# Optimization experiments

Measured on AMD Instinct MI355X. Metric: run time of the kernel, lower is better.

Reference implementation:

```python
import jax, jax.numpy as jnp
import numpy as np

N_NODES = 50000
N_EDGES = 400000
IN_DIM = 128
HID_DIM = 128
OUT_DIM = 128


def setup_inputs() -> dict:
    key = jax.random.key(0)
    k_x, k_e, k_w1, k_b1, k_w2, k_b2 = jax.random.split(key, 6)
    x = jax.random.normal(k_x, (N_NODES, IN_DIM), dtype=jnp.float32)
    edge_index = jax.random.randint(k_e, (2, N_EDGES), 0, N_NODES, dtype=jnp.int64)
    # nn.Linear-style params: W is [out, in], kaiming-uniform-ish init
    lim1 = 1.0 / np.sqrt(IN_DIM)
    lim2 = 1.0 / np.sqrt(HID_DIM)
    W1 = jax.random.uniform(k_w1, (HID_DIM, IN_DIM), jnp.float32, -lim1, lim1)
    b1 = jax.random.uniform(k_b1, (HID_DIM,), jnp.float32, -lim1, lim1)
    W2 = jax.random.uniform(k_w2, (OUT_DIM, HID_DIM), jnp.float32, -lim2, lim2)
    b2 = jax.random.uniform(k_b2, (OUT_DIM,), jnp.float32, -lim2, lim2)
    return {"x": x, "edge_index": edge_index, "W1": W1, "b1": b1, "W2": W2, "b2": b2}


def reference(x, edge_index, W1, b1, W2, b2):
    # h = relu(fc1(x));  dropout in eval mode -> identity
    h = jax.nn.relu(x @ W1.T + b1)                      # [N, hid]
    src, dst = edge_index[0], edge_index[1]
    # gather messages from src, scatter-add (mean) into dst
    agg = jax.ops.segment_sum(h[src], dst, num_segments=N_NODES)      # [N, hid]
    deg = jax.ops.segment_sum(jnp.ones_like(dst, dtype=h.dtype), dst,
                              num_segments=N_NODES)                   # [N]
    deg = jnp.maximum(deg, 1.0)
    agg = agg / deg[:, None]
    # residual add + fc2
    return (agg + h) @ W2.T + b2                        # [N, out]
```

## Files before the change

kernel.cpp:

```cpp
#include <hip/hip_runtime.h>

#define N_NODES 50000
#define N_EDGES 400000
#define DIM 128
#define N_SCAN_BLK ((N_NODES + 255) / 256)

typedef unsigned short u16;
typedef unsigned int   u32;
typedef __bf16 v8bf  __attribute__((ext_vector_type(8)));
typedef float  f32x4 __attribute__((ext_vector_type(4)));
typedef u16    u16x8 __attribute__((ext_vector_type(8)));

union BF8 { u16x8 u; v8bf b; };

__device__ __forceinline__ float bf2f(u16 u) {
    union { u32 i; float f; } v; v.i = ((u32)u) << 16; return v.f;
}
__device__ __forceinline__ u16 f2bf(float f) {
    union { float f; u32 i; } v; v.f = f; u32 u = v.i;
    return (u16)((u + 0x7FFFu + ((u >> 16) & 1u)) >> 16);
}

__global__ __launch_bounds__(256) void cast_w_kernel(
    const float* __restrict__ W1, const float* __restrict__ W2,
    u16* __restrict__ Wb1, u16* __restrict__ Wb2)
{
    int i = blockIdx.x * 256 + threadIdx.x;
    if (i < DIM * DIM) {
        Wb1[i] = f2bf(W1[i]);
        Wb2[i] = f2bf(W2[i]);
    }
}

__global__ __launch_bounds__(256, 3) void fc1_mfma(
    const float* __restrict__ x, const u16* __restrict__ Wb,
    const float* __restrict__ b, u16* __restrict__ h)
{
    __shared__ u16 xs[64 * 136];
    const int t = threadIdx.x;
    const int wave = t >> 6, lane = t & 63, quad = lane >> 4, l15 = lane & 15;
    const int ch = wave >> 1, rh = wave & 1;
    const int row0 = blockIdx.x * 64;

    BF8 barr[4][4];
#pragma unroll
    for (int ct = 0; ct < 4; ++ct)
#pragma unroll
        for (int ks = 0; ks < 4; ++ks)
            barr[ct][ks].u = *(const u16x8*)(
                Wb + (size_t)(ch * 64 + ct * 16 + l15) * DIM + ks * 32 + quad * 8);

    {
        int srow = t >> 2, k0 = (t & 3) * 32;
        int grow = row0 + srow; if (grow >= N_NODES) grow = N_NODES - 1;
        const float* xp = x + (size_t)grow * DIM + k0;
#pragma unroll
        for (int j = 0; j < 4; ++j) {
            float4 f0 = *(const float4*)(xp + j * 8);
            float4 f1 = *(const float4*)(xp + j * 8 + 4);
            u16x8 p;
            p[0] = f2bf(f0.x); p[1] = f2bf(f0.y); p[2] = f2bf(f0.z); p[3] = f2bf(f0.w);
            p[4] = f2bf(f1.x); p[5] = f2bf(f1.y); p[6] = f2bf(f1.z); p[7] = f2bf(f1.w);
            *(u16x8*)&xs[srow * 136 + k0 + j * 8] = p;
        }
    }

    f32x4 acc[2][4];
#pragma unroll
    for (int ct = 0; ct < 4; ++ct) {
        float bv = b[ch * 64 + ct * 16 + l15];
        acc[0][ct] = (f32x4){bv, bv, bv, bv};
        acc[1][ct] = (f32x4){bv, bv, bv, bv};
    }
    __syncthreads();

#pragma unroll
    for (int ks = 0; ks < 4; ++ks) {
        BF8 a0, a1;
        a0.u = *(const u16x8*)&xs[(rh * 32 +  0 + l15) * 136 + ks * 32 + quad * 8];
        a1.u = *(const u16x8*)&xs[(rh * 32 + 16 + l15) * 136 + ks * 32 + quad * 8];
#pragma unroll
        for (int ct = 0; ct < 4; ++ct) {
            acc[0][ct] = __builtin_amdgcn_mfma_f32_16x16x32_bf16(
                a0.b, barr[ct][ks].b, acc[0][ct], 0, 0, 0);
            acc[1][ct] = __builtin_amdgcn_mfma_f32_16x16x32_bf16(
                a1.b, barr[ct][ks].b, acc[1][ct], 0, 0, 0);
        }
    }

#pragma unroll
    for (int rt = 0; rt < 2; ++rt)
#pragma unroll
        for (int i = 0; i < 4; ++i) {
            int row = row0 + rh * 32 + rt * 16 + quad * 4 + i;
            if (row < N_NODES) {
#pragma unroll
                for (int ct = 0; ct < 4; ++ct) {
                    int col = ch * 64 + ct * 16 + l15;
                    h[(size_t)row * DIM + col] = f2bf(fmaxf(acc[rt][ct][i], 0.f));
                }
            }
        }
}

__global__ __launch_bounds__(256, 3) void fc2_mfma(
    const u16* __restrict__ z, const u16* __restrict__ Wb,
    const float* __restrict__ b, float* __restrict__ out)
{
    __shared__ u16 xs[64 * 136];
    const int t = threadIdx.x;
    const int wave = t >> 6, lane = t & 63, quad = lane >> 4, l15 = lane & 15;
    const int ch = wave >> 1, rh = wave & 1;
    const int row0 = blockIdx.x * 64;

    BF8 barr[4][4];
#pragma unroll
    for (int ct = 0; ct < 4; ++ct)
#pragma unroll
        for (int ks = 0; ks < 4; ++ks)
            barr[ct][ks].u = *(const u16x8*)(
                Wb + (size_t)(ch * 64 + ct * 16 + l15) * DIM + ks * 32 + quad * 8);

    {
        int srow = t >> 1, k0 = (t & 1) * 64;
        int grow = row0 + srow; if (grow >= N_NODES) grow = N_NODES - 1;
        const u16* zp = z + (size_t)grow * DIM + k0;
#pragma unroll
        for (int j = 0; j < 8; ++j)
            *(u16x8*)&xs[srow * 136 + k0 + j * 8] = *(const u16x8*)(zp + j * 8);
    }

    f32x4 acc[2][4];
#pragma unroll
    for (int ct = 0; ct < 4; ++ct) {
        float bv = b[ch * 64 + ct * 16 + l15];
        acc[0][ct] = (f32x4){bv, bv, bv, bv};
        acc[1][ct] = (f32x4){bv, bv, bv, bv};
    }
    __syncthreads();

#pragma unroll
    for (int ks = 0; ks < 4; ++ks) {
        BF8 a0, a1;
        a0.u = *(const u16x8*)&xs[(rh * 32 +  0 + l15) * 136 + ks * 32 + quad * 8];
        a1.u = *(const u16x8*)&xs[(rh * 32 + 16 + l15) * 136 + ks * 32 + quad * 8];
#pragma unroll
        for (int ct = 0; ct < 4; ++ct) {
            acc[0][ct] = __builtin_amdgcn_mfma_f32_16x16x32_bf16(
                a0.b, barr[ct][ks].b, acc[0][ct], 0, 0, 0);
            acc[1][ct] = __builtin_amdgcn_mfma_f32_16x16x32_bf16(
                a1.b, barr[ct][ks].b, acc[1][ct], 0, 0, 0);
        }
    }

#pragma unroll
    for (int rt = 0; rt < 2; ++rt)
#pragma unroll
        for (int i = 0; i < 4; ++i) {
            int row = row0 + rh * 32 + rt * 16 + quad * 4 + i;
            if (row < N_NODES) {
#pragma unroll
                for (int ct = 0; ct < 4; ++ct) {
                    int col = ch * 64 + ct * 16 + l15;
                    out[(size_t)row * DIM + col] = acc[rt][ct][i];
                }
            }
        }
}

__global__ __launch_bounds__(256) void count_kernel(
    const int* __restrict__ edst, int* __restrict__ counts)
{
    int e = blockIdx.x * 256 + threadIdx.x;
    if (e >= N_EDGES) return;
    int dst = edst[e];
    if ((unsigned)dst >= N_NODES) return;
    atomicAdd(&counts[dst], 1);
}

__global__ __launch_bounds__(256) void scan_blocks_kernel(
    const int* __restrict__ counts, int* __restrict__ row_ptr,
    int* __restrict__ bsum)
{
    __shared__ int tmp[256];
    const int t = threadIdx.x;
    const int i = blockIdx.x * 256 + t;
    int v = (i < N_NODES) ? counts[i] : 0;
    tmp[t] = v;
    __syncthreads();
#pragma unroll
    for (int ofs = 1; ofs < 256; ofs <<= 1) {
        int add = (t >= ofs) ? tmp[t - ofs] : 0;
        __syncthreads();
        tmp[t] += add;
        __syncthreads();
    }
    if (i < N_NODES) row_ptr[i] = tmp[t] - v;
    if (t == 255) bsum[blockIdx.x] = tmp[255];
}

__global__ __launch_bounds__(256) void scan_top_kernel(
    const int* __restrict__ bsum, int* __restrict__ boff)
{
    __shared__ int tmp[256];
    const int t = threadIdx.x;
    int v = (t < N_SCAN_BLK) ? bsum[t] : 0;
    tmp[t] = v;
    __syncthreads();
#pragma unroll
    for (int ofs = 1; ofs < 256; ofs <<= 1) {
        int add = (t >= ofs) ? tmp[t - ofs] : 0;
        __syncthreads();
        tmp[t] += add;
        __syncthreads();
    }
    if (t < N_SCAN_BLK) boff[t] = tmp[t] - v;
}

__global__ __launch_bounds__(256) void scan_fixup_kernel(
    const int* __restrict__ boff, int* __restrict__ row_ptr,
    int* __restrict__ cursor)
{
    int i = blockIdx.x * 256 + threadIdx.x;
    if (i < N_NODES) {
        int r = row_ptr[i] + boff[blockIdx.x];
        row_ptr[i] = r;
        cursor[i]  = r;
    }
    if (i == 0) row_ptr[N_NODES] = N_EDGES;
}

__global__ __launch_bounds__(256) void bucket_kernel(
    const int* __restrict__ esrc, const int* __restrict__ edst,
    int* __restrict__ cursor, int* __restrict__ esorted)
{
    int e = blockIdx.x * 256 + threadIdx.x;
    if (e >= N_EDGES) return;
    int src = esrc[e], dst = edst[e];
    if ((unsigned)src >= N_NODES || (unsigned)dst >= N_NODES) return;
    int pos = atomicAdd(&cursor[dst], 1);
    esorted[pos] = src;
}

__global__ __launch_bounds__(64) void aggregate_kernel(
    const int* __restrict__ row_ptr, const int* __restrict__ esorted,
    const u16* __restrict__ h, u16* __restrict__ z)
{
    const int n = blockIdx.x;
    const int t = threadIdx.x;
    const int start = row_ptr[n];
    const int end   = row_ptr[n + 1];

    float a0 = 0.f, a1 = 0.f;
    int e = start;
    for (; e + 4 <= end; e += 4) {
        int s0 = esorted[e + 0];
        int s1 = esorted[e + 1];
        int s2 = esorted[e + 2];
        int s3 = esorted[e + 3];
        u32 v0 = *(const u32*)(h + (size_t)s0 * DIM + t * 2);
        u32 v1 = *(const u32*)(h + (size_t)s1 * DIM + t * 2);
        u32 v2 = *(const u32*)(h + (size_t)s2 * DIM + t * 2);
        u32 v3 = *(const u32*)(h + (size_t)s3 * DIM + t * 2);
        a0 += bf2f((u16)v0); a1 += bf2f((u16)(v0 >> 16));
        a0 += bf2f((u16)v1); a1 += bf2f((u16)(v1 >> 16));
        a0 += bf2f((u16)v2); a1 += bf2f((u16)(v2 >> 16));
        a0 += bf2f((u16)v3); a1 += bf2f((u16)(v3 >> 16));
    }
    for (; e < end; ++e) {
        u32 v = *(const u32*)(h + (size_t)esorted[e] * DIM + t * 2);
        a0 += bf2f((u16)v); a1 += bf2f((u16)(v >> 16));
    }

    int deg = end - start;
    float inv = (deg > 0) ? 1.f / (float)deg : 1.f;
    u32 r = *(const u32*)(h + (size_t)n * DIM + t * 2);
    float z0 = a0 * inv + bf2f((u16)r);
    float z1 = a1 * inv + bf2f((u16)(r >> 16));
    u32 p = (u32)f2bf(z0) | ((u32)f2bf(z1) << 16);
    *(u32*)(z + (size_t)n * DIM + t * 2) = p;
}

extern "C" void kernel_launch(void* const* d_in, const int* in_sizes, int n_in,
                              void* d_out, int out_size, void* d_ws, size_t ws_size,
                              hipStream_t stream)
{
    const float* x  = (const float*)d_in[0];
    const int*   ei = (const int*)d_in[1];
    const float* W1 = (const float*)d_in[2];
    const float* b1 = (const float*)d_in[3];
    const float* W2 = (const float*)d_in[4];
    const float* b2 = (const float*)d_in[5];
    float* out = (float*)d_out;

    const int* esrc = ei;
    const int* edst = ei + N_EDGES;

    char* ws = (char*)d_ws;
    size_t off = 0;
    u16* h        = (u16*)(ws + off); off += (size_t)N_NODES * DIM * 2;
    u16* z        = (u16*)(ws + off); off += (size_t)N_NODES * DIM * 2;
    u16* Wb1      = (u16*)(ws + off); off += (size_t)DIM * DIM * 2;
    u16* Wb2      = (u16*)(ws + off); off += (size_t)DIM * DIM * 2;
    int* counts   = (int*)(ws + off); off += (size_t)N_NODES * 4;
    int* row_ptr  = (int*)(ws + off); off += (size_t)(N_NODES + 1) * 4;
    int* cursor   = (int*)(ws + off); off += (size_t)N_NODES * 4;
    int* esorted  = (int*)(ws + off); off += (size_t)N_EDGES * 4;
    int* bsum     = (int*)(ws + off); off += (size_t)N_SCAN_BLK * 4;
    int* boff     = (int*)(ws + off); off += (size_t)N_SCAN_BLK * 4;

    hipMemsetAsync(counts, 0, (size_t)N_NODES * 4, stream);
    cast_w_kernel<<<(DIM * DIM + 255) / 256, 256, 0, stream>>>(W1, W2, Wb1, Wb2);

    fc1_mfma<<<(N_NODES + 63) / 64, 256, 0, stream>>>(x, Wb1, b1, h);
    count_kernel<<<(N_EDGES + 255) / 256, 256, 0, stream>>>(edst, counts);
    scan_blocks_kernel<<<N_SCAN_BLK, 256, 0, stream>>>(counts, row_ptr, bsum);
    scan_top_kernel<<<1, 256, 0, stream>>>(bsum, boff);
    scan_fixup_kernel<<<N_SCAN_BLK, 256, 0, stream>>>(boff, row_ptr, cursor);
    bucket_kernel<<<(N_EDGES + 255) / 256, 256, 0, stream>>>(
        esrc, edst, cursor, esorted);
    aggregate_kernel<<<N_NODES, 64, 0, stream>>>(row_ptr, esorted, h, z);
    fc2_mfma<<<(N_NODES + 63) / 64, 256, 0, stream>>>(z, Wb2, b2, out);
}
```

Before: 181.9 us.

## Fuse CSR build into cooperative kernel and fuse aggregation into fc2

```diff
diff --git a/kernel.cpp b/kernel.cpp
--- a/kernel.cpp
+++ b/kernel.cpp
@@ -1,9 +1,13 @@
 #include <hip/hip_runtime.h>
+#include <hip/hip_cooperative_groups.h>
+
+namespace cg = cooperative_groups;
 
 #define N_NODES 50000
 #define N_EDGES 400000
 #define DIM 128
 #define N_SCAN_BLK ((N_NODES + 255) / 256)
+#define CSR_BLOCKS 512
 
 typedef unsigned short u16;
 typedef unsigned int   u32;
@@ -21,14 +25,82 @@
     return (u16)((u + 0x7FFFu + ((u >> 16) & 1u)) >> 16);
 }
 
-__global__ __launch_bounds__(256) void cast_w_kernel(
+__global__ __launch_bounds__(256) void csr_build(
+    const int* __restrict__ esrc, const int* __restrict__ edst,
     const float* __restrict__ W1, const float* __restrict__ W2,
-    u16* __restrict__ Wb1, u16* __restrict__ Wb2)
+    u16* __restrict__ Wb1, u16* __restrict__ Wb2,
+    int* __restrict__ counts, int* __restrict__ row_ptr,
+    int* __restrict__ cursor, int* __restrict__ esorted,
+    int* __restrict__ bsum, int* __restrict__ boff)
 {
-    int i = blockIdx.x * 256 + threadIdx.x;
-    if (i < DIM * DIM) {
+    cg::grid_group grid = cg::this_grid();
+    __shared__ int tmp[256];
+    const int t   = threadIdx.x;
+    const int bid = blockIdx.x;
+    const int gid = bid * 256 + t;
+    const int G   = CSR_BLOCKS * 256;
+
+    for (int i = gid; i < N_NODES; i += G) counts[i] = 0;
+    for (int i = gid; i < DIM * DIM; i += G) {
         Wb1[i] = f2bf(W1[i]);
         Wb2[i] = f2bf(W2[i]);
+    }
+    grid.sync();
+
+    for (int e = gid; e < N_EDGES; e += G) {
+        int dst = edst[e];
+        if ((unsigned)dst < N_NODES) atomicAdd(&counts[dst], 1);
+    }
+    grid.sync();
+
+    if (bid < N_SCAN_BLK) {
+        int i = bid * 256 + t;
+        int v = (i < N_NODES) ? counts[i] : 0;
+        tmp[t] = v;
+        __syncthreads();
+#pragma unroll
+        for (int ofs = 1; ofs < 256; ofs <<= 1) {
+            int add = (t >= ofs) ? tmp[t - ofs] : 0;
+            __syncthreads();
+            tmp[t] += add;
+            __syncthreads();
+        }
+        if (i < N_NODES) row_ptr[i] = tmp[t] - v;
+        if (t == 255) bsum[bid] = tmp[255];
+    }
+    grid.sync();
+
+    if (bid == 0) {
+        int v = (t < N_SCAN_BLK) ? bsum[t] : 0;
+        tmp[t] = v;
+        __syncthreads();
+#pragma unroll
+        for (int ofs = 1; ofs < 256; ofs <<= 1) {
+            int add = (t >= ofs) ? tmp[t - ofs] : 0;
+            __syncthreads();
+            tmp[t] += add;
+            __syncthreads();
+        }
+        if (t < N_SCAN_BLK) boff[t] = tmp[t] - v;
+    }
+    grid.sync();
+
+    if (bid < N_SCAN_BLK) {
+        int i = bid * 256 + t;
+        if (i < N_NODES) {
+            int r = row_ptr[i] + boff[bid];
+            row_ptr[i] = r;
+            cursor[i]  = r;
+        }
+        if (i == 0) row_ptr[N_NODES] = N_EDGES;
+    }
+    grid.sync();
+
+    for (int e = gid; e < N_EDGES; e += G) {
+        int src = esrc[e], dst = edst[e];
+        if ((unsigned)src >= N_NODES || (unsigned)dst >= N_NODES) continue;
+        int pos = atomicAdd(&cursor[dst], 1);
+        esorted[pos] = src;
     }
 }
 
@@ -103,11 +175,12 @@
         }
 }
 
-__global__ __launch_bounds__(256, 3) void fc2_mfma(
-    const u16* __restrict__ z, const u16* __restrict__ Wb,
+__global__ __launch_bounds__(256, 3) void agg_fc2(
+    const int* __restrict__ row_ptr, const int* __restrict__ esorted,
+    const u16* __restrict__ h, const u16* __restrict__ Wb,
     const float* __restrict__ b, float* __restrict__ out)
 {
-    __shared__ u16 xs[64 * 136];
+    __shared__ u16 zs[64 * 136];
     const int t = threadIdx.x;
     const int wave = t >> 6, lane = t & 63, quad = lane >> 4, l15 = lane & 15;
     const int ch = wave >> 1, rh = wave & 1;
@@ -121,13 +194,41 @@
             barr[ct][ks].u = *(const u16x8*)(
                 Wb + (size_t)(ch * 64 + ct * 16 + l15) * DIM + ks * 32 + quad * 8);
 
-    {
-        int srow = t >> 1, k0 = (t & 1) * 64;
-        int grow = row0 + srow; if (grow >= N_NODES) grow = N_NODES - 1;
-        const u16* zp = z + (size_t)grow * DIM + k0;
-#pragma unroll
-        for (int j = 0; j < 8; ++j)
-            *(u16x8*)&xs[srow * 136 + k0 + j * 8] = *(const u16x8*)(zp + j * 8);
+    for (int i = 0; i < 16; ++i) {
+        int srow = wave * 16 + i;
+        int n = row0 + srow;
+        u32 p = 0;
+        if (n < N_NODES) {
+            const int start = row_ptr[n];
+            const int end   = row_ptr[n + 1];
+            float a0 = 0.f, a1 = 0.f;
+            int e = start;
+            for (; e + 4 <= end; e += 4) {
+                int s0 = esorted[e + 0];
+                int s1 = esorted[e + 1];
+                int s2 = esorted[e + 2];
+                int s3 = esorted[e + 3];
+                u32 v0 = *(const u32*)(h + (size_t)s0 * DIM + lane * 2);
+                u32 v1 = *(const u32*)(h + (size_t)s1 * DIM + lane * 2);
+                u32 v2 = *(const u32*)(h + (size_t)s2 * DIM + lane * 2);
+                u32 v3 = *(const u32*)(h + (size_t)s3 * DIM + lane * 2);
+                a0 += bf2f((u16)v0); a1 += bf2f((u16)(v0 >> 16));
+                a0 += bf2f((u16)v1); a1 += bf2f((u16)(v1 >> 16));
+                a0 += bf2f((u16)v2); a1 += bf2f((u16)(v2 >> 16));
+                a0 += bf2f((u16)v3); a1 += bf2f((u16)(v3 >> 16));
+            }
+            for (; e < end; ++e) {
+                u32 v = *(const u32*)(h + (size_t)esorted[e] * DIM + lane * 2);
+                a0 += bf2f((u16)v); a1 += bf2f((u16)(v >> 16));
+            }
+            int deg = end - start;
+            float inv = (deg > 0) ? 1.f / (float)deg : 1.f;
+            u32 r = *(const u32*)(h + (size_t)n * DIM + lane * 2);
+            float z0 = a0 * inv + bf2f((u16)r);
+            float z1 = a1 * inv + bf2f((u16)(r >> 16));
+            p = (u32)f2bf(z0) | ((u32)f2bf(z1) << 16);
+        }
+        *(u32*)&zs[srow * 136 + lane * 2] = p;
     }
 
     f32x4 acc[2][4];
@@ -142,8 +243,8 @@
 #pragma unroll
     for (int ks = 0; ks < 4; ++ks) {
         BF8 a0, a1;
-        a0.u = *(const u16x8*)&xs[(rh * 32 +  0 + l15) * 136 + ks * 32 + quad * 8];
-        a1.u = *(const u16x8*)&xs[(rh * 32 + 16 + l15) * 136 + ks * 32 + quad * 8];
+        a0.u = *(const u16x8*)&zs[(rh * 32 +  0 + l15) * 136 + ks * 32 + quad * 8];
+        a1.u = *(const u16x8*)&zs[(rh * 32 + 16 + l15) * 136 + ks * 32 + quad * 8];
 #pragma unroll
         for (int ct = 0; ct < 4; ++ct) {
             acc[0][ct] = __builtin_amdgcn_mfma_f32_16x16x32_bf16(
@@ -166,119 +267,6 @@
                 }
             }
         }
-}
-
-__global__ __launch_bounds__(256) void count_kernel(
-    const int* __restrict__ edst, int* __restrict__ counts)
-{
-    int e = blockIdx.x * 256 + threadIdx.x;
-    if (e >= N_EDGES) return;
-    int dst = edst[e];
-    if ((unsigned)dst >= N_NODES) return;
-    atomicAdd(&counts[dst], 1);
-}
-
-__global__ __launch_bounds__(256) void scan_blocks_kernel(
-    const int* __restrict__ counts, int* __restrict__ row_ptr,
-    int* __restrict__ bsum)
-{
-    __shared__ int tmp[256];
-    const int t = threadIdx.x;
-    const int i = blockIdx.x * 256 + t;
-    int v = (i < N_NODES) ? counts[i] : 0;
-    tmp[t] = v;
-    __syncthreads();
-#pragma unroll
-    for (int ofs = 1; ofs < 256; ofs <<= 1) {
-        int add = (t >= ofs) ? tmp[t - ofs] : 0;
-        __syncthreads();
-        tmp[t] += add;
-        __syncthreads();
-    }
-    if (i < N_NODES) row_ptr[i] = tmp[t] - v;
-    if (t == 255) bsum[blockIdx.x] = tmp[255];
-}
-
-__global__ __launch_bounds__(256) void scan_top_kernel(
-    const int* __restrict__ bsum, int* __restrict__ boff)
-{
-    __shared__ int tmp[256];
-    const int t = threadIdx.x;
-    int v = (t < N_SCAN_BLK) ? bsum[t] : 0;
-    tmp[t] = v;
-    __syncthreads();
-#pragma unroll
-    for (int ofs = 1; ofs < 256; ofs <<= 1) {
-        int add = (t >= ofs) ? tmp[t - ofs] : 0;
-        __syncthreads();
-        tmp[t] += add;
-        __syncthreads();
-    }
-    if (t < N_SCAN_BLK) boff[t] = tmp[t] - v;
-}
-
-__global__ __launch_bounds__(256) void scan_fixup_kernel(
-    const int* __restrict__ boff, int* __restrict__ row_ptr,
-    int* __restrict__ cursor)
-{
-    int i = blockIdx.x * 256 + threadIdx.x;
-    if (i < N_NODES) {
-        int r = row_ptr[i] + boff[blockIdx.x];
-        row_ptr[i] = r;
-        cursor[i]  = r;
-    }
-    if (i == 0) row_ptr[N_NODES] = N_EDGES;
-}
-
-__global__ __launch_bounds__(256) void bucket_kernel(
-    const int* __restrict__ esrc, const int* __restrict__ edst,
-    int* __restrict__ cursor, int* __restrict__ esorted)
-{
-    int e = blockIdx.x * 256 + threadIdx.x;
-    if (e >= N_EDGES) return;
-    int src = esrc[e], dst = edst[e];
-    if ((unsigned)src >= N_NODES || (unsigned)dst >= N_NODES) return;
-    int pos = atomicAdd(&cursor[dst], 1);
-    esorted[pos] = src;
-}
-
-__global__ __launch_bounds__(64) void aggregate_kernel(
-    const int* __restrict__ row_ptr, const int* __restrict__ esorted,
-    const u16* __restrict__ h, u16* __restrict__ z)
-{
-    const int n = blockIdx.x;
-    const int t = threadIdx.x;
-    const int start = row_ptr[n];
-    const int end   = row_ptr[n + 1];
-
-    float a0 = 0.f, a1 = 0.f;
-    int e = start;
-    for (; e + 4 <= end; e += 4) {
-        int s0 = esorted[e + 0];
-        int s1 = esorted[e + 1];
-        int s2 = esorted[e + 2];
-        int s3 = esorted[e + 3];
-        u32 v0 = *(const u32*)(h + (size_t)s0 * DIM + t * 2);
-        u32 v1 = *(const u32*)(h + (size_t)s1 * DIM + t * 2);
-        u32 v2 = *(const u32*)(h + (size_t)s2 * DIM + t * 2);
-        u32 v3 = *(const u32*)(h + (size_t)s3 * DIM + t * 2);
-        a0 += bf2f((u16)v0); a1 += bf2f((u16)(v0 >> 16));
-        a0 += bf2f((u16)v1); a1 += bf2f((u16)(v1 >> 16));
-        a0 += bf2f((u16)v2); a1 += bf2f((u16)(v2 >> 16));
-        a0 += bf2f((u16)v3); a1 += bf2f((u16)(v3 >> 16));
-    }
-    for (; e < end; ++e) {
-        u32 v = *(const u32*)(h + (size_t)esorted[e] * DIM + t * 2);
-        a0 += bf2f((u16)v); a1 += bf2f((u16)(v >> 16));
-    }
-
-    int deg = end - start;
-    float inv = (deg > 0) ? 1.f / (float)deg : 1.f;
-    u32 r = *(const u32*)(h + (size_t)n * DIM + t * 2);
-    float z0 = a0 * inv + bf2f((u16)r);
-    float z1 = a1 * inv + bf2f((u16)(r >> 16));
-    u32 p = (u32)f2bf(z0) | ((u32)f2bf(z1) << 16);
-    *(u32*)(z + (size_t)n * DIM + t * 2) = p;
 }
 
 extern "C" void kernel_launch(void* const* d_in, const int* in_sizes, int n_in,
@@ -299,7 +287,6 @@
     char* ws = (char*)d_ws;
     size_t off = 0;
     u16* h        = (u16*)(ws + off); off += (size_t)N_NODES * DIM * 2;
-    u16* z        = (u16*)(ws + off); off += (size_t)N_NODES * DIM * 2;
     u16* Wb1      = (u16*)(ws + off); off += (size_t)DIM * DIM * 2;
     u16* Wb2      = (u16*)(ws + off); off += (size_t)DIM * DIM * 2;
     int* counts   = (int*)(ws + off); off += (size_t)N_NODES * 4;
@@ -309,16 +296,18 @@
     int* bsum     = (int*)(ws + off); off += (size_t)N_SCAN_BLK * 4;
     int* boff     = (int*)(ws + off); off += (size_t)N_SCAN_BLK * 4;
 
-    hipMemsetAsync(counts, 0, (size_t)N_NODES * 4, stream);
-    cast_w_kernel<<<(DIM * DIM + 255) / 256, 256, 0, stream>>>(W1, W2, Wb1, Wb2);
+    {
+        void* args[] = {
+            (void*)&esrc, (void*)&edst, (void*)&W1, (void*)&W2,
+            (void*)&Wb1, (void*)&Wb2, (void*)&counts, (void*)&row_ptr,
+            (void*)&cursor, (void*)&esorted, (void*)&bsum, (void*)&boff
+        };
+        hipLaunchCooperativeKernel((void*)csr_build, dim3(CSR_BLOCKS), dim3(256),
+                                   args, 0, stream);
+    }
 
     fc1_mfma<<<(N_NODES + 63) / 64, 256, 0, stream>>>(x, Wb1, b1, h);
-    count_kernel<<<(N_EDGES + 255) / 256, 256, 0, stream>>>(edst, counts);
-    scan_blocks_kernel<<<N_SCAN_BLK, 256, 0, stream>>>(counts, row_ptr, bsum);
-    scan_top_kernel<<<1, 256, 0, stream>>>(bsum, boff);
-    scan_fixup_kernel<<<N_SCAN_BLK, 256, 0, stream>>>(boff, row_ptr, cursor);
-    bucket_kernel<<<(N_EDGES + 255) / 256, 256, 0, stream>>>(
-        esrc, edst, cursor, esorted);
-    aggregate_kernel<<<N_NODES, 64, 0, stream>>>(row_ptr, esorted, h, z);
-    fc2_mfma<<<(N_NODES + 63) / 64, 256, 0, stream>>>(z, Wb2, b2, out);
-}
+
+    agg_fc2<<<(N_NODES + 63) / 64, 256, 0, stream>>>(
+        row_ptr, esorted, h, Wb2, b2, out);
+}
```

Result: slower. 460.6 us (+153.2%).

## Fuse neighbor aggregation into fc2 kernel and merge count with weight cast

Applied to the files above, without the earlier changes.

```diff
diff --git a/kernel.cpp b/kernel.cpp
--- a/kernel.cpp
+++ b/kernel.cpp
@@ -21,15 +21,90 @@
     return (u16)((u + 0x7FFFu + ((u >> 16) & 1u)) >> 16);
 }
 
-__global__ __launch_bounds__(256) void cast_w_kernel(
+#define EDGE_BLK ((N_EDGES + 255) / 256)
+__global__ __launch_bounds__(256) void count_cast_kernel(
+    const int* __restrict__ edst, int* __restrict__ counts,
     const float* __restrict__ W1, const float* __restrict__ W2,
     u16* __restrict__ Wb1, u16* __restrict__ Wb2)
 {
+    int bid = blockIdx.x;
+    if (bid < EDGE_BLK) {
+        int e = bid * 256 + threadIdx.x;
+        if (e >= N_EDGES) return;
+        int dst = edst[e];
+        if ((unsigned)dst >= N_NODES) return;
+        atomicAdd(&counts[dst], 1);
+    } else {
+        int i = (bid - EDGE_BLK) * 256 + threadIdx.x;
+        if (i < DIM * DIM) {
+            Wb1[i] = f2bf(W1[i]);
+            Wb2[i] = f2bf(W2[i]);
+        }
+    }
+}
+
+__global__ __launch_bounds__(256) void scan_blocks_kernel(
+    const int* __restrict__ counts, int* __restrict__ row_ptr,
+    int* __restrict__ bsum)
+{
+    __shared__ int tmp[256];
+    const int t = threadIdx.x;
+    const int i = blockIdx.x * 256 + t;
+    int v = (i < N_NODES) ? counts[i] : 0;
+    tmp[t] = v;
+    __syncthreads();
+#pragma unroll
+    for (int ofs = 1; ofs < 256; ofs <<= 1) {
+        int add = (t >= ofs) ? tmp[t - ofs] : 0;
+        __syncthreads();
+        tmp[t] += add;
+        __syncthreads();
+    }
+    if (i < N_NODES) row_ptr[i] = tmp[t] - v;
+    if (t == 255) bsum[blockIdx.x] = tmp[255];
+}
+
+__global__ __launch_bounds__(256) void scan_top_kernel(
+    const int* __restrict__ bsum, int* __restrict__ boff)
+{
+    __shared__ int tmp[256];
+    const int t = threadIdx.x;
+    int v = (t < N_SCAN_BLK) ? bsum[t] : 0;
+    tmp[t] = v;
+    __syncthreads();
+#pragma unroll
+    for (int ofs = 1; ofs < 256; ofs <<= 1) {
+        int add = (t >= ofs) ? tmp[t - ofs] : 0;
+        __syncthreads();
+        tmp[t] += add;
+        __syncthreads();
+    }
+    if (t < N_SCAN_BLK) boff[t] = tmp[t] - v;
+}
+
+__global__ __launch_bounds__(256) void scan_fixup_kernel(
+    const int* __restrict__ boff, int* __restrict__ row_ptr,
+    int* __restrict__ cursor)
+{
     int i = blockIdx.x * 256 + threadIdx.x;
-    if (i < DIM * DIM) {
-        Wb1[i] = f2bf(W1[i]);
-        Wb2[i] = f2bf(W2[i]);
-    }
+    if (i < N_NODES) {
+        int r = row_ptr[i] + boff[blockIdx.x];
+        row_ptr[i] = r;
+        cursor[i]  = r;
+    }
+    if (i == 0) row_ptr[N_NODES] = N_EDGES;
+}
+
+__global__ __launch_bounds__(256) void bucket_kernel(
+    const int* __restrict__ esrc, const int* __restrict__ edst,
+    int* __restrict__ cursor, int* __restrict__ esorted)
+{
+    int e = blockIdx.x * 256 + threadIdx.x;
+    if (e >= N_EDGES) return;
+    int src = esrc[e], dst = edst[e];
+    if ((unsigned)src >= N_NODES || (unsigned)dst >= N_NODES) return;
+    int pos = atomicAdd(&cursor[dst], 1);
+    esorted[pos] = src;
 }
 
 __global__ __launch_bounds__(256, 3) void fc1_mfma(
@@ -103,11 +178,12 @@
         }
 }
 
-__global__ __launch_bounds__(256, 3) void fc2_mfma(
-    const u16* __restrict__ z, const u16* __restrict__ Wb,
+__global__ __launch_bounds__(256, 3) void agg_fc2(
+    const int* __restrict__ row_ptr, const int* __restrict__ esorted,
+    const u16* __restrict__ h, const u16* __restrict__ Wb,
     const float* __restrict__ b, float* __restrict__ out)
 {
-    __shared__ u16 xs[64 * 136];
+    __shared__ u16 zs[64 * 136];
     const int t = threadIdx.x;
     const int wave = t >> 6, lane = t & 63, quad = lane >> 4, l15 = lane & 15;
     const int ch = wave >> 1, rh = wave & 1;
@@ -121,13 +197,41 @@
             barr[ct][ks].u = *(const u16x8*)(
                 Wb + (size_t)(ch * 64 + ct * 16 + l15) * DIM + ks * 32 + quad * 8);
 
-    {
-        int srow = t >> 1, k0 = (t & 1) * 64;
-        int grow = row0 + srow; if (grow >= N_NODES) grow = N_NODES - 1;
-        const u16* zp = z + (size_t)grow * DIM + k0;
-#pragma unroll
-        for (int j = 0; j < 8; ++j)
-            *(u16x8*)&xs[srow * 136 + k0 + j * 8] = *(const u16x8*)(zp + j * 8);
+    for (int i = 0; i < 16; ++i) {
+        int srow = wave * 16 + i;
+        int n = row0 + srow;
+        u32 p = 0;
+        if (n < N_NODES) {
+            const int start = row_ptr[n];
+            const int end   = row_ptr[n + 1];
+            float a0 = 0.f, a1 = 0.f;
+            int e = start;
+            for (; e + 4 <= end; e += 4) {
+                int s0 = esorted[e + 0];
+                int s1 = esorted[e + 1];
+                int s2 = esorted[e + 2];
+                int s3 = esorted[e + 3];
+                u32 v0 = *(const u32*)(h + (size_t)s0 * DIM + lane * 2);
+                u32 v1 = *(const u32*)(h + (size_t)s1 * DIM + lane * 2);
+                u32 v2 = *(const u32*)(h + (size_t)s2 * DIM + lane * 2);
+                u32 v3 = *(const u32*)(h + (size_t)s3 * DIM + lane * 2);
+                a0 += bf2f((u16)v0); a1 += bf2f((u16)(v0 >> 16));
+                a0 += bf2f((u16)v1); a1 += bf2f((u16)(v1 >> 16));
+                a0 += bf2f((u16)v2); a1 += bf2f((u16)(v2 >> 16));
+                a0 += bf2f((u16)v3); a1 += bf2f((u16)(v3 >> 16));
+            }
+            for (; e < end; ++e) {
+                u32 v = *(const u32*)(h + (size_t)esorted[e] * DIM + lane * 2);
+                a0 += bf2f((u16)v); a1 += bf2f((u16)(v >> 16));
+            }
+            int deg = end - start;
+            float inv = (deg > 0) ? 1.f / (float)deg : 1.f;
+            u32 r = *(const u32*)(h + (size_t)n * DIM + lane * 2);
+            float z0 = a0 * inv + bf2f((u16)r);
+            float z1 = a1 * inv + bf2f((u16)(r >> 16));
+            p = (u32)f2bf(z0) | ((u32)f2bf(z1) << 16);
+        }
+        *(u32*)&zs[srow * 136 + lane * 2] = p;
     }
 
     f32x4 acc[2][4];
@@ -142,8 +246,8 @@
 #pragma unroll
     for (int ks = 0; ks < 4; ++ks) {
         BF8 a0, a1;
-        a0.u = *(const u16x8*)&xs[(rh * 32 +  0 + l15) * 136 + ks * 32 + quad * 8];
-        a1.u = *(const u16x8*)&xs[(rh * 32 + 16 + l15) * 136 + ks * 32 + quad * 8];
+        a0.u = *(const u16x8*)&zs[(rh * 32 +  0 + l15) * 136 + ks * 32 + quad * 8];
+        a1.u = *(const u16x8*)&zs[(rh * 32 + 16 + l15) * 136 + ks * 32 + quad * 8];
 #pragma unroll
         for (int ct = 0; ct < 4; ++ct) {
             acc[0][ct] = __builtin_amdgcn_mfma_f32_16x16x32_bf16(
@@ -166,119 +270,6 @@
                 }
             }
         }
-}
-
-__global__ __launch_bounds__(256) void count_kernel(
-    const int* __restrict__ edst, int* __restrict__ counts)
-{
-    int e = blockIdx.x * 256 + threadIdx.x;
-    if (e >= N_EDGES) return;
-    int dst = edst[e];
-    if ((unsigned)dst >= N_NODES) return;
-    atomicAdd(&counts[dst], 1);
-}
-
-__global__ __launch_bounds__(256) void scan_blocks_kernel(
-    const int* __restrict__ counts, int* __restrict__ row_ptr,
-    int* __restrict__ bsum)
-{
-    __shared__ int tmp[256];
-    const int t = threadIdx.x;
-    const int i = blockIdx.x * 256 + t;
-    int v = (i < N_NODES) ? counts[i] : 0;
-    tmp[t] = v;
-    __syncthreads();
-#pragma unroll
-    for (int ofs = 1; ofs < 256; ofs <<= 1) {
-        int add = (t >= ofs) ? tmp[t - ofs] : 0;
-        __syncthreads();
-        tmp[t] += add;
-        __syncthreads();
-    }
-    if (i < N_NODES) row_ptr[i] = tmp[t] - v;
-    if (t == 255) bsum[blockIdx.x] = tmp[255];
-}
-
-__global__ __launch_bounds__(256) void scan_top_kernel(
-    const int* __restrict__ bsum, int* __restrict__ boff)
-{
-    __shared__ int tmp[256];
-    const int t = threadIdx.x;
-    int v = (t < N_SCAN_BLK) ? bsum[t] : 0;
-    tmp[t] = v;
-    __syncthreads();
-#pragma unroll
-    for (int ofs = 1; ofs < 256; ofs <<= 1) {
-        int add = (t >= ofs) ? tmp[t - ofs] : 0;
-        __syncthreads();
-        tmp[t] += add;
-        __syncthreads();
-    }
-    if (t < N_SCAN_BLK) boff[t] = tmp[t] - v;
-}
-
-__global__ __launch_bounds__(256) void scan_fixup_kernel(
-    const int* __restrict__ boff, int* __restrict__ row_ptr,
-    int* __restrict__ cursor)
-{
-    int i = blockIdx.x * 256 + threadIdx.x;
-    if (i < N_NODES) {
-        int r = row_ptr[i] + boff[blockIdx.x];
-        row_ptr[i] = r;
-        cursor[i]  = r;
-    }
-    if (i == 0) row_ptr[N_NODES] = N_EDGES;
-}
-
-__global__ __launch_bounds__(256) void bucket_kernel(
-    const int* __restrict__ esrc, const int* __restrict__ edst,
-    int* __restrict__ cursor, int* __restrict__ esorted)
-{
-    int e = blockIdx.x * 256 + threadIdx.x;
-    if (e >= N_EDGES) return;
-    int src = esrc[e], dst = edst[e];
-    if ((unsigned)src >= N_NODES || (unsigned)dst >= N_NODES) return;
-    int pos = atomicAdd(&cursor[dst], 1);
-    esorted[pos] = src;
-}
-
-__global__ __launch_bounds__(64) void aggregate_kernel(
-    const int* __restrict__ row_ptr, const int* __restrict__ esorted,
-    const u16* __restrict__ h, u16* __restrict__ z)
-{
-    const int n = blockIdx.x;
-    const int t = threadIdx.x;
-    const int start = row_ptr[n];
-    const int end   = row_ptr[n + 1];
-
-    float a0 = 0.f, a1 = 0.f;
-    int e = start;
-    for (; e + 4 <= end; e += 4) {
-        int s0 = esorted[e + 0];
-        int s1 = esorted[e + 1];
-        int s2 = esorted[e + 2];
-        int s3 = esorted[e + 3];
-        u32 v0 = *(const u32*)(h + (size_t)s0 * DIM + t * 2);
-        u32 v1 = *(const u32*)(h + (size_t)s1 * DIM + t * 2);
-        u32 v2 = *(const u32*)(h + (size_t)s2 * DIM + t * 2);
-        u32 v3 = *(const u32*)(h + (size_t)s3 * DIM + t * 2);
-        a0 += bf2f((u16)v0); a1 += bf2f((u16)(v0 >> 16));
-        a0 += bf2f((u16)v1); a1 += bf2f((u16)(v1 >> 16));
-        a0 += bf2f((u16)v2); a1 += bf2f((u16)(v2 >> 16));
-        a0 += bf2f((u16)v3); a1 += bf2f((u16)(v3 >> 16));
-    }
-    for (; e < end; ++e) {
-        u32 v = *(const u32*)(h + (size_t)esorted[e] * DIM + t * 2);
-        a0 += bf2f((u16)v); a1 += bf2f((u16)(v >> 16));
-    }
-
-    int deg = end - start;
-    float inv = (deg > 0) ? 1.f / (float)deg : 1.f;
-    u32 r = *(const u32*)(h + (size_t)n * DIM + t * 2);
-    float z0 = a0 * inv + bf2f((u16)r);
-    float z1 = a1 * inv + bf2f((u16)(r >> 16));
-    u32 p = (u32)f2bf(z0) | ((u32)f2bf(z1) << 16);
-    *(u32*)(z + (size_t)n * DIM + t * 2) = p;
 }
 
 extern "C" void kernel_launch(void* const* d_in, const int* in_sizes, int n_in,
@@ -299,7 +290,6 @@
     char* ws = (char*)d_ws;
     size_t off = 0;
     u16* h        = (u16*)(ws + off); off += (size_t)N_NODES * DIM * 2;
-    u16* z        = (u16*)(ws + off); off += (size_t)N_NODES * DIM * 2;
     u16* Wb1      = (u16*)(ws + off); off += (size_t)DIM * DIM * 2;
     u16* Wb2      = (u16*)(ws + off); off += (size_t)DIM * DIM * 2;
     int* counts   = (int*)(ws + off); off += (size_t)N_NODES * 4;
@@ -310,15 +300,15 @@
     int* boff     = (int*)(ws + off); off += (size_t)N_SCAN_BLK * 4;
 
     hipMemsetAsync(counts, 0, (size_t)N_NODES * 4, stream);
-    cast_w_kernel<<<(DIM * DIM + 255) / 256, 256, 0, stream>>>(W1, W2, Wb1, Wb2);
-
-    fc1_mfma<<<(N_NODES + 63) / 64, 256, 0, stream>>>(x, Wb1, b1, h);
-    count_kernel<<<(N_EDGES + 255) / 256, 256, 0, stream>>>(edst, counts);
+    count_cast_kernel<<<EDGE_BLK + 64, 256, 0, stream>>>(
+        edst, counts, W1, W2, Wb1, Wb2);
     scan_blocks_kernel<<<N_SCAN_BLK, 256, 0, stream>>>(counts, row_ptr, bsum);
     scan_top_kernel<<<1, 256, 0, stream>>>(bsum, boff);
     scan_fixup_kernel<<<N_SCAN_BLK, 256, 0, stream>>>(boff, row_ptr, cursor);
     bucket_kernel<<<(N_EDGES + 255) / 256, 256, 0, stream>>>(
         esrc, edst, cursor, esorted);
-    aggregate_kernel<<<N_NODES, 64, 0, stream>>>(row_ptr, esorted, h, z);
-    fc2_mfma<<<(N_NODES + 63) / 64, 256, 0, stream>>>(z, Wb2, b2, out);
-}
+
+    fc1_mfma<<<(N_NODES + 63) / 64, 256, 0, stream>>>(x, Wb1, b1, h);
+    agg_fc2<<<(N_NODES + 63) / 64, 256, 0, stream>>>(
+        row_ptr, esorted, h, Wb2, b2, out);
+}
```

After: 201.6 us. 1.11x slower.
